# Kernel optimization log

Measured on AMD Instinct MI355X. Metric: run time of the kernel, lower is better.

## Reference

```python
import jax, jax.numpy as jnp
import numpy as np


def setup_inputs() -> dict:
    key = jax.random.key(0)
    k1, k2 = jax.random.split(key)
    B, C, T = 8, 64, 65536  # batch, channels, sequence length (power of 2)
    x = jax.random.normal(k1, (B, C, T), dtype=jnp.float32)
    h = jax.random.normal(k2, (B, C, T), dtype=jnp.float32)
    return {"x": x, "h": h}


def reference(x, h):
    """Causal (linear) convolution of x with kernel h via FFT, truncated to
    the input length — the math computed by FlashFFTConv. The original module
    casts the signal x to bfloat16 before the conv (kernel h stays fp32); we
    mimic that quantization, then compute the FFT in fp32."""
    T = x.shape[-1]
    n = 2 * T  # zero-pad to 2T so circular conv == linear causal conv on [0, T)
    xb = x.astype(jnp.bfloat16).astype(jnp.float32)  # bf16 quantization of signal
    X = jnp.fft.rfft(xb, n=n)          # (B, C, T+1) complex64
    H = jnp.fft.rfft(h, n=n)           # (B, C, T+1) complex64
    y = jnp.fft.irfft(X * H, n=n)[..., :T]  # causal output, same length as x
    return y.astype(jnp.float32)
```

## Files before the change

### kernel.cpp

```cpp
#include <hip/hip_runtime.h>
#include <hip/hip_bf16.h>
#include <hip/hip_fp16.h>
#include <math.h>


#define TLEN 65536
#define NFFT 131072
#define NN1 512
#define NN2 256

#define WFENCE() asm volatile("s_waitcnt lgkmcnt(0)" ::: "memory")

__device__ __forceinline__ float2 cmul(float2 a, float2 b) {
  return make_float2(a.x * b.x - a.y * b.y, a.x * b.y + a.y * b.x);
}
__device__ __forceinline__ float2 cadd(float2 a, float2 b) { return make_float2(a.x + b.x, a.y + b.y); }
__device__ __forceinline__ float2 csub(float2 a, float2 b) { return make_float2(a.x - b.x, a.y - b.y); }

template <int S>
__device__ __forceinline__ void fft8(float2 v[8]) {
  const float C = 0.70710678118654752f;
  const float s = (float)S;
  float2 b0 = cadd(v[0], v[4]), b4 = csub(v[0], v[4]);
  float2 b1 = cadd(v[1], v[5]), d1 = csub(v[1], v[5]);
  float2 b2 = cadd(v[2], v[6]), d2 = csub(v[2], v[6]);
  float2 b3 = cadd(v[3], v[7]), d3 = csub(v[3], v[7]);
  float2 b5 = make_float2(C * (d1.x - s * d1.y), C * (s * d1.x + d1.y));
  float2 b6 = make_float2(-s * d2.y, s * d2.x);
  float2 b7 = make_float2(C * (-d3.x - s * d3.y), C * (s * d3.x - d3.y));
  float2 c0 = cadd(b0, b2), c2 = csub(b0, b2);
  float2 c1 = cadd(b1, b3), e3 = csub(b1, b3);
  float2 c3 = make_float2(-s * e3.y, s * e3.x);
  float2 c4 = cadd(b4, b6), c6 = csub(b4, b6);
  float2 c5 = cadd(b5, b7), e7 = csub(b5, b7);
  float2 c7 = make_float2(-s * e7.y, s * e7.x);
  v[0] = cadd(c0, c1); v[4] = csub(c0, c1);
  v[2] = cadd(c2, c3); v[6] = csub(c2, c3);
  v[1] = cadd(c4, c5); v[5] = csub(c4, c5);
  v[3] = cadd(c6, c7); v[7] = csub(c6, c7);
}

template <int S>
__device__ __forceinline__ void fft4(float2 v[4]) {
  const float s = (float)S;
  float2 t0 = cadd(v[0], v[2]), t1 = csub(v[0], v[2]);
  float2 t2 = cadd(v[1], v[3]), t3 = csub(v[1], v[3]);
  float2 it3 = make_float2(-s * t3.y, s * t3.x);
  v[0] = cadd(t0, t2); v[2] = csub(t0, t2);
  v[1] = cadd(t1, it3); v[3] = csub(t1, it3);
}

__global__ void k_init_tw(float2* __restrict__ tw) {
  int m = blockIdx.x * 256 + threadIdx.x;
  double ang = (double)m * (-2.0 * 3.14159265358979323846 / (double)NFFT);
  tw[m] = make_float2((float)cos(ang), (float)sin(ang));
}

__global__ __launch_bounds__(256, 3) void k_fwd_inner(
    const float* __restrict__ x, const float* __restrict__ h,
    __half2* __restrict__ buf, const float2* __restrict__ tw) {
  __shared__ __half2 tz[128 * 18];
  __shared__ float2 xch[4 * 512];
  __shared__ __half2 to[256 * 17];
  __shared__ float2 w256[256];
  const int tid = threadIdx.x;
  const int lane = tid & 63;
  const int wid = tid >> 6;
  const int s = blockIdx.x >> 5;
  const int n1b = (blockIdx.x & 31) * 16;
  w256[tid] = tw[tid * (NFFT / 256)];
  const float* xp = x + (size_t)s * TLEN;
  const float* hp = h + (size_t)s * TLEN;
  {
    int a = tid & 3, q = tid >> 2;
#pragma unroll
    for (int iter = 0; iter < 2; ++iter) {
      int n2 = q + 64 * iter;
      size_t gi = (size_t)(n1b + 4 * a) + (size_t)512 * n2;
      float4 xv = *(const float4*)(xp + gi);
      float4 hv = *(const float4*)(hp + gi);
      float xs[4] = {xv.x, xv.y, xv.z, xv.w};
      float hs[4] = {hv.x, hv.y, hv.z, hv.w};
#pragma unroll
      for (int c = 0; c < 4; ++c) {
        float xb = __bfloat162float(__float2bfloat16(xs[c]));
        tz[18 * n2 + 4 * a + c] = __float22half2_rn(make_float2(xb, hs[c]));
      }
    }
  }
  __syncthreads();
  float2* X = xch + wid * 512;
  const int f = lane >> 5;
  const int l5 = lane & 31;
  const int fb = f * 256;
  const int hh = l5 >> 2, bb = l5 & 3;
#pragma unroll
  for (int p2 = 0; p2 < 2; ++p2) {
    const int n1l = 8 * p2 + 2 * wid + f;
    const int n1 = n1b + n1l;
    float2 v[8];
#pragma unroll
    for (int j = 0; j < 4; ++j) v[j] = __half22float2(tz[18 * (32 * j + l5) + n1l]);
#pragma unroll
    for (int j = 4; j < 8; ++j) v[j] = make_float2(0.f, 0.f);
    fft8<-1>(v);
    { float2 w1 = w256[l5]; float2 pw = w1;
#pragma unroll
      for (int k0 = 1; k0 < 8; ++k0) { v[k0] = cmul(v[k0], pw); pw = cmul(pw, w1); } }
#pragma unroll
    for (int k0 = 0; k0 < 8; ++k0) X[fb + 32 * k0 + (l5 ^ (4 * k0))] = v[k0];
    WFENCE();
#pragma unroll
    for (int j2 = 0; j2 < 8; ++j2) v[j2] = X[fb + 32 * hh + ((4 * j2 + bb) ^ (4 * hh))];
    fft8<-1>(v);
    { float2 w1 = w256[8 * bb]; float2 pw = w1;
#pragma unroll
      for (int kp = 1; kp < 8; ++kp) { v[kp] = cmul(v[kp], pw); pw = cmul(pw, w1); } }
    WFENCE();
#pragma unroll
    for (int kp = 0; kp < 8; ++kp) {
      int cc = kp & 3, gg = kp >> 2;
      X[fb + 128 * gg + 32 * cc + 8 * (bb ^ cc) + hh] = v[kp];
    }
    WFENCE();
#pragma unroll
    for (int g = 0; g < 2; ++g) {
      float2 u4[4];
#pragma unroll
      for (int t = 0; t < 4; ++t) u4[t] = X[fb + 128 * g + 32 * bb + 8 * (t ^ bb) + hh];
      fft4<-1>(u4);
#pragma unroll
      for (int k1q = 0; k1q < 4; ++k1q) {
        int k2 = hh + 8 * bb + 32 * g + 64 * k1q;
        float ang = (float)(n1 * k2) * (6.28318530717958647692f / (float)NFFT);
        float sn, cs; __sincosf(ang, &sn, &cs);
        float2 y = cmul(u4[k1q], make_float2(cs, -sn));
        to[17 * k2 + n1l] = __float22half2_rn(y);
      }
    }
    WFENCE();
  }
  __syncthreads();
  {
    int c = tid & 3, q = tid >> 2;
#pragma unroll
    for (int iter = 0; iter < 4; ++iter) {
      int row = q + 64 * iter;
      __half2 h0 = to[17 * row + 4 * c + 0], h1 = to[17 * row + 4 * c + 1];
      __half2 h2 = to[17 * row + 4 * c + 2], h3 = to[17 * row + 4 * c + 3];
      int4 pk;
      pk.x = *(int*)&h0; pk.y = *(int*)&h1; pk.z = *(int*)&h2; pk.w = *(int*)&h3;
      *(int4*)(buf + ((size_t)s * NN2 + row) * NN1 + n1b + 4 * c) = pk;
    }
  }
}

__global__ __launch_bounds__(256, 6) void k_mid(
    __half2* __restrict__ buf, const float2* __restrict__ tw) {
  __shared__ float2 smem[4 * 576 + 512];
  float2* w512 = smem + 4 * 576;
  const int tid = threadIdx.x;
  const int lane = tid & 63;
  const int wid = tid >> 6;
  const int s = blockIdx.x >> 6;
  const int pb = blockIdx.x & 63;
  for (int i = tid; i < 512; i += 256) w512[i] = tw[i * (NFFT / NN1)];
  const int p = 2 * pb + (wid >> 1);
  const int cidx = wid & 1;
  const int k2 = (p == 0) ? (cidx ? 128 : 0) : (cidx ? 256 - p : p);
  const int c = k2;
  const bool selfA = (p == 0 && cidx == 0);
  float2* R = smem + wid * 576;
  float2* PR = smem + ((p == 0) ? wid : (wid ^ 1)) * 576;
  __half2* colp = buf + ((size_t)s * NN2 + c) * NN1;

  float2 v[8];
#pragma unroll
  for (int k = 0; k < 8; ++k) v[k] = __half22float2(colp[lane + 64 * k]);
  __syncthreads();

  const int jm = lane >> 3, mo = lane & 7;
  const int kbase = jm + 8 * mo;

  fft8<-1>(v);
  { float2 w1 = w512[lane]; float2 pw = w1;
#pragma unroll
    for (int j = 1; j < 8; ++j) { v[j] = cmul(v[j], pw); pw = cmul(pw, w1); } }
#pragma unroll
  for (int j = 0; j < 8; ++j) R[64 * j + (lane ^ (8 * j))] = v[j];
  WFENCE();
#pragma unroll
  for (int m1 = 0; m1 < 8; ++m1) v[m1] = R[64 * jm + ((mo + 8 * m1) ^ (8 * jm))];
  fft8<-1>(v);
  { float2 w1 = w512[8 * mo]; float2 pw = w1;
#pragma unroll
    for (int r0 = 1; r0 < 8; ++r0) { v[r0] = cmul(v[r0], pw); pw = cmul(pw, w1); } }
  WFENCE();
#pragma unroll
  for (int r0 = 0; r0 < 8; ++r0) R[9 * (8 * jm + r0) + mo] = v[r0];
  WFENCE();
#pragma unroll
  for (int m0 = 0; m0 < 8; ++m0) v[m0] = R[9 * lane + m0];
  fft8<-1>(v);

  WFENCE();
#pragma unroll
  for (int r1 = 0; r1 < 8; ++r1) { int k = kbase + 64 * r1; R[k + (k >> 3)] = v[r1]; }
  __syncthreads();
  float2 z2[8];
#pragma unroll
  for (int r1 = 0; r1 < 8; ++r1) {
    int k = kbase + 64 * r1;
    int pk = selfA ? ((512 - k) & 511) : (511 - k);
    z2[r1] = PR[pk + (pk >> 3)];
  }
  __syncthreads();
#pragma unroll
  for (int r1 = 0; r1 < 8; ++r1) {
    float2 z1 = v[r1], q = z2[r1];
    float2 Xf = make_float2(0.5f * (z1.x + q.x), 0.5f * (z1.y - q.y));
    float2 Hf = make_float2(0.5f * (z1.y + q.y), 0.5f * (q.x - z1.x));
    v[r1] = cmul(Xf, Hf);
  }
#pragma unroll
  for (int r1 = 0; r1 < 8; ++r1) { int k = kbase + 64 * r1; R[k + (k >> 3)] = v[r1]; }
  WFENCE();
#pragma unroll
  for (int kk = 0; kk < 8; ++kk) { int ci = lane + 64 * kk; v[kk] = R[ci + (ci >> 3)]; }

  fft8<1>(v);
  { float2 w1 = w512[lane]; w1.y = -w1.y; float2 pw = w1;
#pragma unroll
    for (int j = 1; j < 8; ++j) { v[j] = cmul(v[j], pw); pw = cmul(pw, w1); } }
  WFENCE();
#pragma unroll
  for (int j = 0; j < 8; ++j) R[64 * j + (lane ^ (8 * j))] = v[j];
  WFENCE();
#pragma unroll
  for (int m1 = 0; m1 < 8; ++m1) v[m1] = R[64 * jm + ((mo + 8 * m1) ^ (8 * jm))];
  fft8<1>(v);
  { float2 w1 = w512[8 * mo]; w1.y = -w1.y; float2 pw = w1;
#pragma unroll
    for (int r0 = 1; r0 < 8; ++r0) { v[r0] = cmul(v[r0], pw); pw = cmul(pw, w1); } }
  WFENCE();
#pragma unroll
  for (int r0 = 0; r0 < 8; ++r0) R[9 * (8 * jm + r0) + mo] = v[r0];
  WFENCE();
#pragma unroll
  for (int m0 = 0; m0 < 8; ++m0) v[m0] = R[9 * lane + m0];
  fft8<1>(v);

  const float invN = 1.0f / (float)NFFT;
  const float w0 = 6.28318530717958647692f / (float)NFFT;
  WFENCE();
#pragma unroll
  for (int r1 = 0; r1 < 8; ++r1) {
    int n1 = kbase + 64 * r1;
    float ang = (float)(n1 * k2) * w0;
    float sn, cs; __sincosf(ang, &sn, &cs);
    float2 y = cmul(v[r1], make_float2(cs, sn));
    R[n1 + (n1 >> 3)] = make_float2(y.x * invN, y.y * invN);
  }
  WFENCE();
#pragma unroll
  for (int u = 0; u < 8; ++u) {
    int ci = lane + 64 * u;
    colp[ci] = __float22half2_rn(R[ci + (ci >> 3)]);
  }
}

__global__ __launch_bounds__(256, 3) void k_inv_outer(
    const __half2* __restrict__ buf, float* __restrict__ out,
    const float2* __restrict__ tw) {
  __shared__ __half2 ti[16 * 257];
  __shared__ float2 xch[4 * 512];
  __shared__ float ty[128 * 17];
  __shared__ float2 w256[256];
  const int tid = threadIdx.x;
  const int lane = tid & 63;
  const int wid = tid >> 6;
  const int s = blockIdx.x >> 5;
  const int n1b = (blockIdx.x & 31) * 16;
  w256[tid] = tw[tid * (NFFT / 256)];
  {
    int c = tid & 3, q = tid >> 2;
#pragma unroll
    for (int iter = 0; iter < 4; ++iter) {
      int row = q + 64 * iter;
      int4 pk = *(const int4*)(buf + ((size_t)s * NN2 + row) * NN1 + n1b + 4 * c);
      __half2 hv[4];
      *(int*)&hv[0] = pk.x; *(int*)&hv[1] = pk.y; *(int*)&hv[2] = pk.z; *(int*)&hv[3] = pk.w;
#pragma unroll
      for (int j = 0; j < 4; ++j) ti[(4 * c + j) * 257 + row] = hv[j];
    }
  }
  __syncthreads();
  float2* X = xch + wid * 512;
  const int f = lane >> 5;
  const int l5 = lane & 31;
  const int fb = f * 256;
  const int hh = l5 >> 2, bb = l5 & 3;
#pragma unroll
  for (int p2 = 0; p2 < 2; ++p2) {
    const int n1l = 8 * p2 + 2 * wid + f;
    float2 v2[2][4];
#pragma unroll
    for (int g = 0; g < 2; ++g)
#pragma unroll
      for (int k1q = 0; k1q < 4; ++k1q)
        v2[g][k1q] = __half22float2(ti[n1l * 257 + hh + 8 * bb + 32 * g + 64 * k1q]);
#pragma unroll
    for (int g = 0; g < 2; ++g) fft4<1>(v2[g]);
#pragma unroll
    for (int g = 0; g < 2; ++g)
#pragma unroll
      for (int t = 0; t < 4; ++t)
        X[fb + 128 * g + 32 * bb + 8 * (t ^ bb) + hh] = v2[g][t];
    WFENCE();
    float2 v[8];
#pragma unroll
    for (int kp = 0; kp < 8; ++kp) {
      int cc = kp & 3, gg = kp >> 2;
      v[kp] = X[fb + 128 * gg + 32 * cc + 8 * (bb ^ cc) + hh];
    }
    { float2 w1 = w256[8 * bb]; w1.y = -w1.y; float2 pw = w1;
#pragma unroll
      for (int kp = 1; kp < 8; ++kp) { v[kp] = cmul(v[kp], pw); pw = cmul(pw, w1); } }
    fft8<1>(v);
    WFENCE();
#pragma unroll
    for (int j2 = 0; j2 < 8; ++j2) X[fb + 32 * hh + ((4 * j2 + bb) ^ (4 * hh))] = v[j2];
    WFENCE();
#pragma unroll
    for (int k0 = 0; k0 < 8; ++k0) v[k0] = X[fb + 32 * k0 + (l5 ^ (4 * k0))];
    { float2 w1 = w256[l5]; w1.y = -w1.y; float2 pw = w1;
#pragma unroll
      for (int k0 = 1; k0 < 8; ++k0) { v[k0] = cmul(v[k0], pw); pw = cmul(pw, w1); } }
    fft8<1>(v);
#pragma unroll
    for (int j = 0; j < 4; ++j) ty[17 * (32 * j + l5) + n1l] = v[j].x;
    WFENCE();
  }
  __syncthreads();
  {
    int e = tid & 1, n2 = tid >> 1;
    float* op = out + (size_t)s * TLEN + (size_t)512 * n2 + n1b + 8 * e;
    float4 o0, o1;
    o0.x = ty[17 * n2 + 8 * e + 0]; o0.y = ty[17 * n2 + 8 * e + 1];
    o0.z = ty[17 * n2 + 8 * e + 2]; o0.w = ty[17 * n2 + 8 * e + 3];
    o1.x = ty[17 * n2 + 8 * e + 4]; o1.y = ty[17 * n2 + 8 * e + 5];
    o1.z = ty[17 * n2 + 8 * e + 6]; o1.w = ty[17 * n2 + 8 * e + 7];
    *(float4*)op = o0;
    *(float4*)(op + 4) = o1;
  }
}

extern "C" void kernel_launch(void* const* d_in, const int* in_sizes, int n_in,
                              void* d_out, int out_size, void* d_ws, size_t ws_size,
                              hipStream_t stream) {
  (void)n_in; (void)out_size; (void)ws_size;
  const float* x = (const float*)d_in[0];
  const float* h = (const float*)d_in[1];
  float* out = (float*)d_out;
  float2* tw = (float2*)d_ws;
  __half2* buf = (__half2*)((char*)d_ws + (size_t)(2 * 1024 * 1024));
  int seqs = in_sizes[0] / TLEN;
  k_init_tw<<<NFFT / 256, 256, 0, stream>>>(tw);
  k_fwd_inner<<<seqs * 32, 256, 0, stream>>>(x, h, buf, tw);
  k_mid<<<seqs * 64, 256, 0, stream>>>(buf, tw);
  k_inv_outer<<<seqs * 32, 256, 0, stream>>>(buf, out, tw);
}
```

Before: 678.4 us.

## Use packed f32 VALU ops for complex math and recurrence-based twiddles

```diff
diff --git a/kernel.cpp b/kernel.cpp
--- a/kernel.cpp
+++ b/kernel.cpp
@@ -11,29 +11,76 @@
 
 #define WFENCE() asm volatile("s_waitcnt lgkmcnt(0)" ::: "memory")
 
-__device__ __forceinline__ float2 cmul(float2 a, float2 b) {
-  return make_float2(a.x * b.x - a.y * b.y, a.x * b.y + a.y * b.x);
-}
-__device__ __forceinline__ float2 cadd(float2 a, float2 b) { return make_float2(a.x + b.x, a.y + b.y); }
-__device__ __forceinline__ float2 csub(float2 a, float2 b) { return make_float2(a.x - b.x, a.y - b.y); }
+typedef float cpx __attribute__((ext_vector_type(2)));
+
+static __device__ __forceinline__ cpx mkc(float a, float b) { cpx r; r.x = a; r.y = b; return r; }
+static __device__ __forceinline__ cpx h2c(__half2 h) { float2 f = __half22float2(h); return mkc(f.x, f.y); }
+static __device__ __forceinline__ __half2 c2h(cpx c) { return __float22half2_rn(make_float2(c.x, c.y)); }
+
+static __device__ __forceinline__ cpx cadd(cpx a, cpx b) {
+  cpx d; asm("v_pk_add_f32 %0, %1, %2" : "=v"(d) : "v"(a), "v"(b)); return d;
+}
+static __device__ __forceinline__ cpx csub(cpx a, cpx b) {
+  cpx d; asm("v_pk_add_f32 %0, %1, %2 neg_lo:[0,1] neg_hi:[0,1]" : "=v"(d) : "v"(a), "v"(b)); return d;
+}
+static __device__ __forceinline__ cpx cscale(cpx a, cpx c) {
+  cpx d; asm("v_pk_mul_f32 %0, %1, %2" : "=v"(d) : "v"(a), "v"(c)); return d;
+}
+static __device__ __forceinline__ cpx cmul(cpx a, cpx b) {
+  cpx t, d;
+  asm("v_pk_mul_f32 %0, %1, %2 op_sel:[0,0] op_sel_hi:[0,1]" : "=v"(t) : "v"(a), "v"(b));
+  asm("v_pk_fma_f32 %0, %1, %2, %3 op_sel:[1,1,0] op_sel_hi:[1,0,1] neg_lo:[1,0,0]"
+      : "=v"(d) : "v"(a), "v"(b), "v"(t));
+  return d;
+}
+static __device__ __forceinline__ cpx cmulc(cpx a, cpx b) {
+  cpx t, d;
+  asm("v_pk_mul_f32 %0, %1, %2 op_sel:[0,0] op_sel_hi:[0,1]" : "=v"(t) : "v"(a), "v"(b));
+  asm("v_pk_fma_f32 %0, %1, %2, %3 op_sel:[1,1,0] op_sel_hi:[1,0,1] neg_hi:[0,0,1]"
+      : "=v"(d) : "v"(a), "v"(b), "v"(t));
+  return d;
+}
+template <int S> static __device__ __forceinline__ cpx cmuli(cpx a) {
+  cpx z = mkc(0.f, 0.f); cpx d;
+  if constexpr (S == 1)
+    asm("v_pk_add_f32 %0, %1, %2 op_sel:[1,0] op_sel_hi:[0,0] neg_lo:[1,0]" : "=v"(d) : "v"(a), "v"(z));
+  else
+    asm("v_pk_add_f32 %0, %1, %2 op_sel:[1,0] op_sel_hi:[0,0] neg_hi:[1,0]" : "=v"(d) : "v"(a), "v"(z));
+  return d;
+}
+template <int S> static __device__ __forceinline__ cpx cw1(cpx d, cpx Cc) {
+  cpx u;
+  if constexpr (S == -1)
+    asm("v_pk_add_f32 %0, %1, %1 op_sel:[0,1] op_sel_hi:[1,0] neg_hi:[0,1]" : "=v"(u) : "v"(d));
+  else
+    asm("v_pk_add_f32 %0, %1, %1 op_sel:[0,1] op_sel_hi:[0,1] neg_lo:[0,1]" : "=v"(u) : "v"(d));
+  return cscale(u, Cc);
+}
+template <int S> static __device__ __forceinline__ cpx cw3(cpx d, cpx Cc) {
+  cpx u;
+  if constexpr (S == -1)
+    asm("v_pk_add_f32 %0, %1, %1 op_sel:[1,0] op_sel_hi:[0,1] neg_lo:[0,1] neg_hi:[1,1]" : "=v"(u) : "v"(d));
+  else
+    asm("v_pk_add_f32 %0, %1, %1 op_sel:[0,1] op_sel_hi:[0,1] neg_lo:[1,1] neg_hi:[0,1]" : "=v"(u) : "v"(d));
+  return cscale(u, Cc);
+}
 
 template <int S>
-__device__ __forceinline__ void fft8(float2 v[8]) {
-  const float C = 0.70710678118654752f;
-  const float s = (float)S;
-  float2 b0 = cadd(v[0], v[4]), b4 = csub(v[0], v[4]);
-  float2 b1 = cadd(v[1], v[5]), d1 = csub(v[1], v[5]);
-  float2 b2 = cadd(v[2], v[6]), d2 = csub(v[2], v[6]);
-  float2 b3 = cadd(v[3], v[7]), d3 = csub(v[3], v[7]);
-  float2 b5 = make_float2(C * (d1.x - s * d1.y), C * (s * d1.x + d1.y));
-  float2 b6 = make_float2(-s * d2.y, s * d2.x);
-  float2 b7 = make_float2(C * (-d3.x - s * d3.y), C * (s * d3.x - d3.y));
-  float2 c0 = cadd(b0, b2), c2 = csub(b0, b2);
-  float2 c1 = cadd(b1, b3), e3 = csub(b1, b3);
-  float2 c3 = make_float2(-s * e3.y, s * e3.x);
-  float2 c4 = cadd(b4, b6), c6 = csub(b4, b6);
-  float2 c5 = cadd(b5, b7), e7 = csub(b5, b7);
-  float2 c7 = make_float2(-s * e7.y, s * e7.x);
+__device__ __forceinline__ void fft8(cpx v[8]) {
+  cpx Cc; Cc.x = 0.70710678118654752f; Cc.y = 0.70710678118654752f;
+  cpx b0 = cadd(v[0], v[4]), b4 = csub(v[0], v[4]);
+  cpx b1 = cadd(v[1], v[5]), d1 = csub(v[1], v[5]);
+  cpx b2 = cadd(v[2], v[6]), d2 = csub(v[2], v[6]);
+  cpx b3 = cadd(v[3], v[7]), d3 = csub(v[3], v[7]);
+  cpx b5 = cw1<S>(d1, Cc);
+  cpx b6 = cmuli<S>(d2);
+  cpx b7 = cw3<S>(d3, Cc);
+  cpx c0 = cadd(b0, b2), c2 = csub(b0, b2);
+  cpx c1 = cadd(b1, b3), e3 = csub(b1, b3);
+  cpx c3 = cmuli<S>(e3);
+  cpx c4 = cadd(b4, b6), c6 = csub(b4, b6);
+  cpx c5 = cadd(b5, b7), e7 = csub(b5, b7);
+  cpx c7 = cmuli<S>(e7);
   v[0] = cadd(c0, c1); v[4] = csub(c0, c1);
   v[2] = cadd(c2, c3); v[6] = csub(c2, c3);
   v[1] = cadd(c4, c5); v[5] = csub(c4, c5);
@@ -41,28 +88,27 @@
 }
 
 template <int S>
-__device__ __forceinline__ void fft4(float2 v[4]) {
-  const float s = (float)S;
-  float2 t0 = cadd(v[0], v[2]), t1 = csub(v[0], v[2]);
-  float2 t2 = cadd(v[1], v[3]), t3 = csub(v[1], v[3]);
-  float2 it3 = make_float2(-s * t3.y, s * t3.x);
+__device__ __forceinline__ void fft4(cpx v[4]) {
+  cpx t0 = cadd(v[0], v[2]), t1 = csub(v[0], v[2]);
+  cpx t2 = cadd(v[1], v[3]), t3 = csub(v[1], v[3]);
+  cpx it3 = cmuli<S>(t3);
   v[0] = cadd(t0, t2); v[2] = csub(t0, t2);
   v[1] = cadd(t1, it3); v[3] = csub(t1, it3);
 }
 
-__global__ void k_init_tw(float2* __restrict__ tw) {
+__global__ void k_init_tw(cpx* __restrict__ tw) {
   int m = blockIdx.x * 256 + threadIdx.x;
   double ang = (double)m * (-2.0 * 3.14159265358979323846 / (double)NFFT);
-  tw[m] = make_float2((float)cos(ang), (float)sin(ang));
+  tw[m] = mkc((float)cos(ang), (float)sin(ang));
 }
 
 __global__ __launch_bounds__(256, 3) void k_fwd_inner(
     const float* __restrict__ x, const float* __restrict__ h,
-    __half2* __restrict__ buf, const float2* __restrict__ tw) {
+    __half2* __restrict__ buf, const cpx* __restrict__ tw) {
   __shared__ __half2 tz[128 * 18];
-  __shared__ float2 xch[4 * 512];
+  __shared__ cpx xch[4 * 512];
   __shared__ __half2 to[256 * 17];
-  __shared__ float2 w256[256];
+  __shared__ cpx w256[256];
   const int tid = threadIdx.x;
   const int lane = tid & 63;
   const int wid = tid >> 6;
@@ -89,7 +135,7 @@
     }
   }
   __syncthreads();
-  float2* X = xch + wid * 512;
+  cpx* X = xch + wid * 512;
   const int f = lane >> 5;
   const int l5 = lane & 31;
   const int fb = f * 256;
@@ -98,13 +144,15 @@
   for (int p2 = 0; p2 < 2; ++p2) {
     const int n1l = 8 * p2 + 2 * wid + f;
     const int n1 = n1b + n1l;
-    float2 v[8];
-#pragma unroll
-    for (int j = 0; j < 4; ++j) v[j] = __half22float2(tz[18 * (32 * j + l5) + n1l]);
-#pragma unroll
-    for (int j = 4; j < 8; ++j) v[j] = make_float2(0.f, 0.f);
+    cpx tbase = tw[n1 * (hh + 8 * bb)];
+    cpx tstep = tw[32 * n1];
+    cpx v[8];
+#pragma unroll
+    for (int j = 0; j < 4; ++j) v[j] = h2c(tz[18 * (32 * j + l5) + n1l]);
+#pragma unroll
+    for (int j = 4; j < 8; ++j) v[j] = mkc(0.f, 0.f);
     fft8<-1>(v);
-    { float2 w1 = w256[l5]; float2 pw = w1;
+    { cpx w1 = w256[l5]; cpx pw = w1;
 #pragma unroll
       for (int k0 = 1; k0 < 8; ++k0) { v[k0] = cmul(v[k0], pw); pw = cmul(pw, w1); } }
 #pragma unroll
@@ -113,7 +161,7 @@
 #pragma unroll
     for (int j2 = 0; j2 < 8; ++j2) v[j2] = X[fb + 32 * hh + ((4 * j2 + bb) ^ (4 * hh))];
     fft8<-1>(v);
-    { float2 w1 = w256[8 * bb]; float2 pw = w1;
+    { cpx w1 = w256[8 * bb]; cpx pw = w1;
 #pragma unroll
       for (int kp = 1; kp < 8; ++kp) { v[kp] = cmul(v[kp], pw); pw = cmul(pw, w1); } }
     WFENCE();
@@ -123,19 +171,20 @@
       X[fb + 128 * gg + 32 * cc + 8 * (bb ^ cc) + hh] = v[kp];
     }
     WFENCE();
+    cpx tstep2 = cmul(tstep, tstep);
 #pragma unroll
     for (int g = 0; g < 2; ++g) {
-      float2 u4[4];
+      cpx u4[4];
 #pragma unroll
       for (int t = 0; t < 4; ++t) u4[t] = X[fb + 128 * g + 32 * bb + 8 * (t ^ bb) + hh];
       fft4<-1>(u4);
+      cpx wg = (g == 0) ? tbase : cmul(tbase, tstep);
 #pragma unroll
       for (int k1q = 0; k1q < 4; ++k1q) {
         int k2 = hh + 8 * bb + 32 * g + 64 * k1q;
-        float ang = (float)(n1 * k2) * (6.28318530717958647692f / (float)NFFT);
-        float sn, cs; __sincosf(ang, &sn, &cs);
-        float2 y = cmul(u4[k1q], make_float2(cs, -sn));
-        to[17 * k2 + n1l] = __float22half2_rn(y);
+        cpx y = cmul(u4[k1q], wg);
+        to[17 * k2 + n1l] = c2h(y);
+        wg = cmul(wg, tstep2);
       }
     }
     WFENCE();
@@ -147,18 +196,18 @@
     for (int iter = 0; iter < 4; ++iter) {
       int row = q + 64 * iter;
       __half2 h0 = to[17 * row + 4 * c + 0], h1 = to[17 * row + 4 * c + 1];
-      __half2 h2 = to[17 * row + 4 * c + 2], h3 = to[17 * row + 4 * c + 3];
+      __half2 h2v = to[17 * row + 4 * c + 2], h3 = to[17 * row + 4 * c + 3];
       int4 pk;
-      pk.x = *(int*)&h0; pk.y = *(int*)&h1; pk.z = *(int*)&h2; pk.w = *(int*)&h3;
+      pk.x = *(int*)&h0; pk.y = *(int*)&h1; pk.z = *(int*)&h2v; pk.w = *(int*)&h3;
       *(int4*)(buf + ((size_t)s * NN2 + row) * NN1 + n1b + 4 * c) = pk;
     }
   }
 }
 
 __global__ __launch_bounds__(256, 6) void k_mid(
-    __half2* __restrict__ buf, const float2* __restrict__ tw) {
-  __shared__ float2 smem[4 * 576 + 512];
-  float2* w512 = smem + 4 * 576;
+    __half2* __restrict__ buf, const cpx* __restrict__ tw) {
+  __shared__ cpx smem[4 * 576 + 512];
+  cpx* w512 = smem + 4 * 576;
   const int tid = threadIdx.x;
   const int lane = tid & 63;
   const int wid = tid >> 6;
@@ -170,20 +219,23 @@
   const int k2 = (p == 0) ? (cidx ? 128 : 0) : (cidx ? 256 - p : p);
   const int c = k2;
   const bool selfA = (p == 0 && cidx == 0);
-  float2* R = smem + wid * 576;
-  float2* PR = smem + ((p == 0) ? wid : (wid ^ 1)) * 576;
+  cpx* R = smem + wid * 576;
+  cpx* PR = smem + ((p == 0) ? wid : (wid ^ 1)) * 576;
   __half2* colp = buf + ((size_t)s * NN2 + c) * NN1;
-
-  float2 v[8];
-#pragma unroll
-  for (int k = 0; k < 8; ++k) v[k] = __half22float2(colp[lane + 64 * k]);
-  __syncthreads();
 
   const int jm = lane >> 3, mo = lane & 7;
   const int kbase = jm + 8 * mo;
+  const float invN4 = 0.25f / (float)NFFT;
+  cpx tbase = cscale(tw[kbase * k2], mkc(invN4, invN4));
+  cpx tstep = tw[64 * k2];
+
+  cpx v[8];
+#pragma unroll
+  for (int k = 0; k < 8; ++k) v[k] = h2c(colp[lane + 64 * k]);
+  __syncthreads();
 
   fft8<-1>(v);
-  { float2 w1 = w512[lane]; float2 pw = w1;
+  { cpx w1 = w512[lane]; cpx pw = w1;
 #pragma unroll
     for (int j = 1; j < 8; ++j) { v[j] = cmul(v[j], pw); pw = cmul(pw, w1); } }
 #pragma unroll
@@ -192,7 +244,7 @@
 #pragma unroll
   for (int m1 = 0; m1 < 8; ++m1) v[m1] = R[64 * jm + ((mo + 8 * m1) ^ (8 * jm))];
   fft8<-1>(v);
-  { float2 w1 = w512[8 * mo]; float2 pw = w1;
+  { cpx w1 = w512[8 * mo]; cpx pw = w1;
 #pragma unroll
     for (int r0 = 1; r0 < 8; ++r0) { v[r0] = cmul(v[r0], pw); pw = cmul(pw, w1); } }
   WFENCE();
@@ -207,7 +259,7 @@
 #pragma unroll
   for (int r1 = 0; r1 < 8; ++r1) { int k = kbase + 64 * r1; R[k + (k >> 3)] = v[r1]; }
   __syncthreads();
-  float2 z2[8];
+  cpx z2[8];
 #pragma unroll
   for (int r1 = 0; r1 < 8; ++r1) {
     int k = kbase + 64 * r1;
@@ -217,10 +269,11 @@
   __syncthreads();
 #pragma unroll
   for (int r1 = 0; r1 < 8; ++r1) {
-    float2 z1 = v[r1], q = z2[r1];
-    float2 Xf = make_float2(0.5f * (z1.x + q.x), 0.5f * (z1.y - q.y));
-    float2 Hf = make_float2(0.5f * (z1.y + q.y), 0.5f * (q.x - z1.x));
-    v[r1] = cmul(Xf, Hf);
+    cpx z1 = v[r1], q = z2[r1];
+    cpx Xf2, Hf2;
+    asm("v_pk_add_f32 %0, %1, %2 neg_hi:[0,1]" : "=v"(Xf2) : "v"(z1), "v"(q));
+    asm("v_pk_add_f32 %0, %1, %2 op_sel:[1,1] op_sel_hi:[0,0] neg_hi:[1,0]" : "=v"(Hf2) : "v"(z1), "v"(q));
+    v[r1] = cmul(Xf2, Hf2);
   }
 #pragma unroll
   for (int r1 = 0; r1 < 8; ++r1) { int k = kbase + 64 * r1; R[k + (k >> 3)] = v[r1]; }
@@ -229,7 +282,7 @@
   for (int kk = 0; kk < 8; ++kk) { int ci = lane + 64 * kk; v[kk] = R[ci + (ci >> 3)]; }
 
   fft8<1>(v);
-  { float2 w1 = w512[lane]; w1.y = -w1.y; float2 pw = w1;
+  { cpx w1 = w512[lane]; w1.y = -w1.y; cpx pw = w1;
 #pragma unroll
     for (int j = 1; j < 8; ++j) { v[j] = cmul(v[j], pw); pw = cmul(pw, w1); } }
   WFENCE();
@@ -239,7 +292,7 @@
 #pragma unroll
   for (int m1 = 0; m1 < 8; ++m1) v[m1] = R[64 * jm + ((mo + 8 * m1) ^ (8 * jm))];
   fft8<1>(v);
-  { float2 w1 = w512[8 * mo]; w1.y = -w1.y; float2 pw = w1;
+  { cpx w1 = w512[8 * mo]; w1.y = -w1.y; cpx pw = w1;
 #pragma unroll
     for (int r0 = 1; r0 < 8; ++r0) { v[r0] = cmul(v[r0], pw); pw = cmul(pw, w1); } }
   WFENCE();
@@ -250,32 +303,29 @@
   for (int m0 = 0; m0 < 8; ++m0) v[m0] = R[9 * lane + m0];
   fft8<1>(v);
 
-  const float invN = 1.0f / (float)NFFT;
-  const float w0 = 6.28318530717958647692f / (float)NFFT;
   WFENCE();
 #pragma unroll
   for (int r1 = 0; r1 < 8; ++r1) {
     int n1 = kbase + 64 * r1;
-    float ang = (float)(n1 * k2) * w0;
-    float sn, cs; __sincosf(ang, &sn, &cs);
-    float2 y = cmul(v[r1], make_float2(cs, sn));
-    R[n1 + (n1 >> 3)] = make_float2(y.x * invN, y.y * invN);
+    cpx y = cmulc(v[r1], tbase);
+    R[n1 + (n1 >> 3)] = y;
+    tbase = cmul(tbase, tstep);
   }
   WFENCE();
 #pragma unroll
   for (int u = 0; u < 8; ++u) {
     int ci = lane + 64 * u;
-    colp[ci] = __float22half2_rn(R[ci + (ci >> 3)]);
+    colp[ci] = c2h(R[ci + (ci >> 3)]);
   }
 }
 
 __global__ __launch_bounds__(256, 3) void k_inv_outer(
     const __half2* __restrict__ buf, float* __restrict__ out,
-    const float2* __restrict__ tw) {
+    const cpx* __restrict__ tw) {
   __shared__ __half2 ti[16 * 257];
-  __shared__ float2 xch[4 * 512];
+  __shared__ cpx xch[4 * 512];
   __shared__ float ty[128 * 17];
-  __shared__ float2 w256[256];
+  __shared__ cpx w256[256];
   const int tid = threadIdx.x;
   const int lane = tid & 63;
   const int wid = tid >> 6;
@@ -295,7 +345,7 @@
     }
   }
   __syncthreads();
-  float2* X = xch + wid * 512;
+  cpx* X = xch + wid * 512;
   const int f = lane >> 5;
   const int l5 = lane & 31;
   const int fb = f * 256;
@@ -303,12 +353,12 @@
 #pragma unroll
   for (int p2 = 0; p2 < 2; ++p2) {
     const int n1l = 8 * p2 + 2 * wid + f;
-    float2 v2[2][4];
+    cpx v2[2][4];
 #pragma unroll
     for (int g = 0; g < 2; ++g)
 #pragma unroll
       for (int k1q = 0; k1q < 4; ++k1q)
-        v2[g][k1q] = __half22float2(ti[n1l * 257 + hh + 8 * bb + 32 * g + 64 * k1q]);
+        v2[g][k1q] = h2c(ti[n1l * 257 + hh + 8 * bb + 32 * g + 64 * k1q]);
 #pragma unroll
     for (int g = 0; g < 2; ++g) fft4<1>(v2[g]);
 #pragma unroll
@@ -317,13 +367,13 @@
       for (int t = 0; t < 4; ++t)
         X[fb + 128 * g + 32 * bb + 8 * (t ^ bb) + hh] = v2[g][t];
     WFENCE();
-    float2 v[8];
+    cpx v[8];
 #pragma unroll
     for (int kp = 0; kp < 8; ++kp) {
       int cc = kp & 3, gg = kp >> 2;
       v[kp] = X[fb + 128 * gg + 32 * cc + 8 * (bb ^ cc) + hh];
     }
-    { float2 w1 = w256[8 * bb]; w1.y = -w1.y; float2 pw = w1;
+    { cpx w1 = w256[8 * bb]; w1.y = -w1.y; cpx pw = w1;
 #pragma unroll
       for (int kp = 1; kp < 8; ++kp) { v[kp] = cmul(v[kp], pw); pw = cmul(pw, w1); } }
     fft8<1>(v);
@@ -333,7 +383,7 @@
     WFENCE();
 #pragma unroll
     for (int k0 = 0; k0 < 8; ++k0) v[k0] = X[fb + 32 * k0 + (l5 ^ (4 * k0))];
-    { float2 w1 = w256[l5]; w1.y = -w1.y; float2 pw = w1;
+    { cpx w1 = w256[l5]; w1.y = -w1.y; cpx pw = w1;
 #pragma unroll
       for (int k0 = 1; k0 < 8; ++k0) { v[k0] = cmul(v[k0], pw); pw = cmul(pw, w1); } }
     fft8<1>(v);
@@ -362,7 +412,7 @@
   const float* x = (const float*)d_in[0];
   const float* h = (const float*)d_in[1];
   float* out = (float*)d_out;
-  float2* tw = (float2*)d_ws;
+  cpx* tw = (cpx*)d_ws;
   __half2* buf = (__half2*)((char*)d_ws + (size_t)(2 * 1024 * 1024));
   int seqs = in_sizes[0] / TLEN;
   k_init_tw<<<NFFT / 256, 256, 0, stream>>>(tw);
```

Result: slower. 698.8 us (+3.0%).
